# Performance work log

Hardware: AMD Instinct MI355X
Metric: run time of the kernel (lower is better)

The kernel has to match this reference:

```python
import jax, jax.numpy as jnp
import numpy as np

N, E = 20000, 160000
NODE_DIM, EDGE_DIM, H, STEPS = 64, 16, 32, 3


def setup_inputs() -> dict:
    key = jax.random.key(0)
    ks = jax.random.split(key, 10)
    node_feat = jax.random.normal(ks[0], (N, NODE_DIM), dtype=jnp.float32)
    edge_index = jax.random.randint(ks[1], (2, E), 0, N, dtype=jnp.int32)
    edge_feat = jax.random.normal(ks[2], (E, EDGE_DIM), dtype=jnp.float32)
    # node_proj: Linear(node_dim, hidden)
    W_np = jax.random.normal(ks[3], (H, NODE_DIM), dtype=jnp.float32) / np.sqrt(NODE_DIM)
    b_np = jnp.zeros((H,), dtype=jnp.float32)
    # edge_net: Linear(edge_dim, hidden*hidden) -> reshape [E, H, H]
    W_e = jax.random.normal(ks[4], (H * H, EDGE_DIM), dtype=jnp.float32) / np.sqrt(EDGE_DIM)
    b_e = jnp.zeros((H * H,), dtype=jnp.float32)
    # GRUCell params (torch layout: [3H, H], gate order r, z, n)
    W_ih = jax.random.normal(ks[5], (3 * H, H), dtype=jnp.float32) / np.sqrt(H)
    W_hh = jax.random.normal(ks[6], (3 * H, H), dtype=jnp.float32) / np.sqrt(H)
    b_ih = jnp.zeros((3 * H,), dtype=jnp.float32)
    b_hh = jnp.zeros((3 * H,), dtype=jnp.float32)
    return {
        "node_feat": node_feat, "edge_index": edge_index, "edge_feat": edge_feat,
        "W_np": W_np, "b_np": b_np, "W_e": W_e, "b_e": b_e,
        "W_ih": W_ih, "W_hh": W_hh, "b_ih": b_ih, "b_hh": b_hh,
    }


def _gru_cell(x, h, W_ih, W_hh, b_ih, b_hh):
    gi = x @ W_ih.T + b_ih  # [N, 3H]
    gh = h @ W_hh.T + b_hh
    ir, iz, inn = jnp.split(gi, 3, axis=-1)
    hr, hz, hn = jnp.split(gh, 3, axis=-1)
    r = jax.nn.sigmoid(ir + hr)
    z = jax.nn.sigmoid(iz + hz)
    n = jnp.tanh(inn + r * hn)
    return (1.0 - z) * n + z * h


def reference(node_feat, edge_index, edge_feat, W_np, b_np, W_e, b_e, W_ih, W_hh, b_ih, b_hh):
    h = node_feat @ W_np.T + b_np                      # [N, H]
    A = (edge_feat @ W_e.T + b_e).reshape(-1, H, H)    # [E, H, H] per-edge matrices
    src, dst = edge_index[0], edge_index[1]
    for _ in range(STEPS):
        # m[v] += A[e] @ h[src[e]]  -> batched matvec + scatter-add
        msg = jnp.einsum('ehk,ek->eh', A, h[src])      # [E, H]
        m = jax.ops.segment_sum(msg, dst, num_segments=N)
        h = _gru_cell(m, h, W_ih, W_hh, b_ih, b_hh)
    return h
```

## Files before the change

### kernel.cpp

```cpp
#include <hip/hip_runtime.h>
#include <math.h>

#define N_NODES 20000
#define N_EDGES 160000
#define NODE_DIM 64
#define EDGE_DIM 16
#define H 32
#define STEPS 3

__global__ void hist_src_kernel(const int* __restrict__ ei, int* __restrict__ deg) {
    int e = blockIdx.x * 256 + threadIdx.x;
    if (e < N_EDGES) atomicAdd(&deg[ei[e]], 1);
}

__global__ void scan_a_kernel(const int* __restrict__ deg,
                              int* __restrict__ part, int* __restrict__ bsum) {
    __shared__ int s[256];
    int v = blockIdx.x * 256 + threadIdx.x;
    int x = (v < N_NODES) ? deg[v] : 0;
    s[threadIdx.x] = x;
    __syncthreads();
    for (int off = 1; off < 256; off <<= 1) {
        int t = (threadIdx.x >= off) ? s[threadIdx.x - off] : 0;
        __syncthreads();
        s[threadIdx.x] += t;
        __syncthreads();
    }
    if (v < N_NODES) part[v] = s[threadIdx.x] - x;
    if (threadIdx.x == 255) bsum[blockIdx.x] = s[255];
}

__global__ void scan_b_kernel(int* __restrict__ rowptr,
                              const int* __restrict__ bsum,
                              int* __restrict__ cursor) {
    __shared__ int boff[80];
    if (threadIdx.x == 0) {
        int run = 0;
        for (int b = 0; b < 79; ++b) { boff[b] = run; run += bsum[b]; }
    }
    __syncthreads();
    for (int v = threadIdx.x; v < N_NODES; v += 256) {
        int r = rowptr[v] + boff[v >> 8];
        rowptr[v] = r;
        cursor[v] = r;
    }
    if (threadIdx.x == 0) rowptr[N_NODES] = N_EDGES;
}

__global__ void fill_src_kernel(const int* __restrict__ ei, int* __restrict__ cursor,
                                int* __restrict__ eperm, int2* __restrict__ sd2) {
    int e = blockIdx.x * 256 + threadIdx.x;
    if (e < N_EDGES) {
        int s = ei[e];
        int slot = atomicAdd(&cursor[s], 1);
        eperm[slot] = e;
        sd2[slot]   = make_int2(s, ei[N_EDGES + e]);
    }
}

__global__ void permute_ef_kernel(const float* __restrict__ ef,
                                  const int* __restrict__ eperm,
                                  float* __restrict__ ef2) {
    int t = blockIdx.x * 256 + threadIdx.x;
    if (t < N_EDGES * EDGE_DIM) {
        int j = t >> 4;
        int d = t & 15;
        ef2[t] = ef[eperm[j] * EDGE_DIM + d];
    }
}

__global__ void node_proj_kernel(const float* __restrict__ nf,
                                 const float* __restrict__ W,
                                 const float* __restrict__ b,
                                 float* __restrict__ h) {
    int tid = blockIdx.x * blockDim.x + threadIdx.x;
    if (tid >= N_NODES * H) return;
    int v = tid >> 5;
    int i = tid & 31;
    const float* __restrict__ row = nf + v * NODE_DIM;
    const float* __restrict__ w   = W + i * NODE_DIM;
    float acc = b[i];
#pragma unroll
    for (int d = 0; d < NODE_DIM; ++d) acc = fmaf(row[d], w[d], acc);
    h[tid] = acc;
}

__global__ __launch_bounds__(576)
void fused_msg_kernel(const float* __restrict__ We,
                      const float* __restrict__ be,
                      const float* __restrict__ h,
                      const int* __restrict__ rowptr,
                      const int2* __restrict__ sd2,
                      const float* __restrict__ ef2,
                      float* __restrict__ m) {
    __shared__ float hs[16 * 32];
    __shared__ float Ul[16 * 576];

    int t = threadIdx.x;

    float wreg[32];
    int p = -1;
    if (t < 512) {
        int L = t >> 4, q = (t >> 2) & 3, e = t & 3;
        int d = t & 15;
#pragma unroll
        for (int k = 0; k < H; ++k) wreg[k] = We[(L * H + k) * EDGE_DIM + d];
        p = q * 136 + L * 4 + e;
    } else if (t < 544) {
        int i = t - 512;
#pragma unroll
        for (int k = 0; k < H; ++k) wreg[k] = be[i * H + k];
        p = 544 + i;
    }

    int v0 = blockIdx.x * 16;

    if (t < 512) hs[t] = h[(size_t)v0 * H + t];
    __syncthreads();

    if (p >= 0) {
        for (int n = 0; n < 16; n += 2) {
            const float4* __restrict__ hp0 = (const float4*)(hs + n * H);
            const float4* __restrict__ hp1 = (const float4*)(hs + (n + 1) * H);
            float a0 = 0.f, a1 = 0.f;
#pragma unroll
            for (int kk = 0; kk < 8; ++kk) {
                float4 q0 = hp0[kk];
                float4 q1 = hp1[kk];
                a0 = fmaf(wreg[4 * kk + 0], q0.x, a0);
                a1 = fmaf(wreg[4 * kk + 0], q1.x, a1);
                a0 = fmaf(wreg[4 * kk + 1], q0.y, a0);
                a1 = fmaf(wreg[4 * kk + 1], q1.y, a1);
                a0 = fmaf(wreg[4 * kk + 2], q0.z, a0);
                a1 = fmaf(wreg[4 * kk + 2], q1.z, a1);
                a0 = fmaf(wreg[4 * kk + 3], q0.w, a0);
                a1 = fmaf(wreg[4 * kk + 3], q1.w, a1);
            }
            Ul[n * 576 + p]       = a0;
            Ul[(n + 1) * 576 + p] = a1;
        }
    }
    __syncthreads();

    int hw    = t >> 5;
    int lane  = t & 31;
    int jbeg  = rowptr[v0];
    int jend  = rowptr[v0 + 16];
    int nE    = jend - jbeg;
    int chunk = (nE + 17) / 18;
    int ja    = jbeg + hw * chunk;
    int jz    = ja + chunk; if (jz > jend) jz = jend;

    if (ja < jz) {
        int s_prev = -1;
        float4 u0 = {0,0,0,0}, u1 = {0,0,0,0}, u2 = {0,0,0,0}, u3 = {0,0,0,0};
        float  bv = 0.f;

        int2 sd = sd2[ja];
        const float4* __restrict__ ep0 = (const float4*)(ef2 + (size_t)ja * EDGE_DIM);
        float4 e0 = ep0[0], e1 = ep0[1], e2 = ep0[2], e3 = ep0[3];

        for (int j = ja; j < jz; ++j) {
            int jn = (j + 1 < jz) ? (j + 1) : j;
            int2 sdn = sd2[jn];
            const float4* __restrict__ epn =
                (const float4*)(ef2 + (size_t)jn * EDGE_DIM);
            float4 f0 = epn[0], f1 = epn[1], f2 = epn[2], f3 = epn[3];

            if (sd.x != s_prev) {
                s_prev = sd.x;
                int ls = sd.x - v0;
                const float4* __restrict__ up = (const float4*)(Ul + ls * 576);
                u0 = up[0 * 34 + lane];
                u1 = up[1 * 34 + lane];
                u2 = up[2 * 34 + lane];
                u3 = up[3 * 34 + lane];
                bv = Ul[ls * 576 + 544 + lane];
            }

            float msg = bv;
            msg = fmaf(e0.x, u0.x, msg);
            msg = fmaf(e0.y, u0.y, msg);
            msg = fmaf(e0.z, u0.z, msg);
            msg = fmaf(e0.w, u0.w, msg);
            msg = fmaf(e1.x, u1.x, msg);
            msg = fmaf(e1.y, u1.y, msg);
            msg = fmaf(e1.z, u1.z, msg);
            msg = fmaf(e1.w, u1.w, msg);
            msg = fmaf(e2.x, u2.x, msg);
            msg = fmaf(e2.y, u2.y, msg);
            msg = fmaf(e2.z, u2.z, msg);
            msg = fmaf(e2.w, u2.w, msg);
            msg = fmaf(e3.x, u3.x, msg);
            msg = fmaf(e3.y, u3.y, msg);
            msg = fmaf(e3.z, u3.z, msg);
            msg = fmaf(e3.w, u3.w, msg);

            atomicAdd(&m[(size_t)sd.y * H + lane], msg);

            sd = sdn;
            e0 = f0; e1 = f1; e2 = f2; e3 = f3;
        }
    }
}

__global__ __launch_bounds__(256, 4)
void gru_kernel(const float* __restrict__ Wih,
                const float* __restrict__ Whh,
                const float* __restrict__ bih,
                const float* __restrict__ bhh,
                float* __restrict__ m,
                const float* __restrict__ h,
                float* __restrict__ hout) {
    __shared__ float xs[16 * 64];
    __shared__ float gs[16 * 32 * 5];

    int c = threadIdx.x & 127;
    float4 wc[16];
    if (c < 96) {
        const float4* p = (const float4*)(Wih + c * H);
#pragma unroll
        for (int q = 0; q < 8; ++q) wc[q] = p[q];
    } else {
#pragma unroll
        for (int q = 0; q < 8; ++q) wc[q] = make_float4(0.f, 0.f, 0.f, 0.f);
    }
    int hrow = (c < 64) ? c : ((c >= 96) ? (c - 32) : -1);
    if (hrow >= 0) {
        const float4* p = (const float4*)(Whh + hrow * H);
#pragma unroll
        for (int q = 0; q < 8; ++q) wc[8 + q] = p[q];
    } else {
#pragma unroll
        for (int q = 0; q < 8; ++q) wc[8 + q] = make_float4(0.f, 0.f, 0.f, 0.f);
    }
    float bias;
    if (c < 64)      bias = bih[c] + bhh[c];
    else if (c < 96) bias = bih[c];
    else             bias = bhh[c - 32];

    int g    = threadIdx.x >> 5;
    int lane = threadIdx.x & 31;
    int half = threadIdx.x >> 7;
    int ci   = c & 31;
    int gt   = c >> 5;

    int v0 = blockIdx.x * 16;
    {
#pragma unroll
        for (int nn = 0; nn < 2; ++nn) {
            int n = g + nn * 8;
            int v = v0 + n;
            float mv = m[(size_t)v * H + lane];
            m[(size_t)v * H + lane] = 0.f;
            xs[n * 64 + lane]      = mv;
            xs[n * 64 + 32 + lane] = h[(size_t)v * H + lane];
        }
        __syncthreads();

#pragma unroll
        for (int n = 0; n < 8; n += 2) {
            const float4* x0 = (const float4*)(xs + (half * 8 + n) * 64);
            const float4* x1 = (const float4*)(xs + (half * 8 + n + 1) * 64);
            float acc0 = bias, acc1 = bias;
#pragma unroll
            for (int q = 0; q < 16; ++q) {
                float4 w = wc[q];
                float4 a = x0[q];
                float4 b = x1[q];
                acc0 = fmaf(w.x, a.x, acc0); acc1 = fmaf(w.x, b.x, acc1);
                acc0 = fmaf(w.y, a.y, acc0); acc1 = fmaf(w.y, b.y, acc1);
                acc0 = fmaf(w.z, a.z, acc0); acc1 = fmaf(w.z, b.z, acc1);
                acc0 = fmaf(w.w, a.w, acc0); acc1 = fmaf(w.w, b.w, acc1);
            }
            gs[((half * 8 + n)     * 32 + ci) * 5 + gt] = acc0;
            gs[((half * 8 + n + 1) * 32 + ci) * 5 + gt] = acc1;
        }
        __syncthreads();

        for (int t = threadIdx.x; t < 16 * 32; t += 256) {
            int nl = t >> 5, ii = t & 31;
            const float* gp = gs + (size_t)t * 5;
            float rs = gp[0], zs = gp[1], in_ = gp[2], hn = gp[3];
            float hv = xs[nl * 64 + 32 + ii];
            float r   = 1.f / (1.f + __expf(-rs));
            float z   = 1.f / (1.f + __expf(-zs));
            float nn2 = tanhf(in_ + r * hn);
            hout[(size_t)(v0 + nl) * H + ii] = (1.f - z) * nn2 + z * hv;
        }
    }
}

extern "C" void kernel_launch(void* const* d_in, const int* in_sizes, int n_in,
                              void* d_out, int out_size, void* d_ws, size_t ws_size,
                              hipStream_t stream) {
    const float* node_feat = (const float*)d_in[0];
    const int*   edge_idx  = (const int*)  d_in[1];
    const float* edge_feat = (const float*)d_in[2];
    const float* W_np      = (const float*)d_in[3];
    const float* b_np      = (const float*)d_in[4];
    const float* W_e       = (const float*)d_in[5];
    const float* b_e       = (const float*)d_in[6];
    const float* W_ih      = (const float*)d_in[7];
    const float* W_hh      = (const float*)d_in[8];
    const float* b_ih      = (const float*)d_in[9];
    const float* b_hh      = (const float*)d_in[10];

    float* h      = (float*)d_ws;
    float* m      = h + (size_t)N_NODES * H;
    float* ef2    = m + (size_t)N_NODES * H;
    int* rowptr   = (int*)(ef2 + (size_t)N_EDGES * EDGE_DIM);
    int* cursor   = rowptr + (N_NODES + 1);
    int* bsum     = cursor + N_NODES;
    int* eperm    = bsum + 80;
    int2* sd2     = (int2*)(eperm + N_EDGES);
    float* out    = (float*)d_out;

    hipMemsetAsync(m, 0, (size_t)N_NODES * H * sizeof(float), stream);
    hipMemsetAsync(cursor, 0, N_NODES * sizeof(int), stream);
    hist_src_kernel<<<(N_EDGES + 255) / 256, 256, 0, stream>>>(edge_idx, cursor);
    scan_a_kernel<<<(N_NODES + 255) / 256, 256, 0, stream>>>(cursor, rowptr, bsum);
    scan_b_kernel<<<1, 256, 0, stream>>>(rowptr, bsum, cursor);
    fill_src_kernel<<<(N_EDGES + 255) / 256, 256, 0, stream>>>(edge_idx, cursor,
                                                               eperm, sd2);
    permute_ef_kernel<<<(N_EDGES * EDGE_DIM + 255) / 256, 256, 0, stream>>>(
        edge_feat, eperm, ef2);

    node_proj_kernel<<<(N_NODES * H + 255) / 256, 256, 0, stream>>>(
        node_feat, W_np, b_np, h);

    for (int step = 0; step < STEPS; ++step) {
        fused_msg_kernel<<<N_NODES / 16, 576, 0, stream>>>(
            W_e, b_e, h, rowptr, sd2, ef2, m);
        float* dst_h = (step == STEPS - 1) ? out : h;
        gru_kernel<<<N_NODES / 16, 256, 0, stream>>>(W_ih, W_hh, b_ih, b_hh,
                                                     m, h, dst_h);
    }
}
```

Before: 302.8 us.

## Fuse setup kernels into one cooperative kernel; process two node tiles per message block

Replaces the two memsets and six preprocessing kernels with a single cooperative setup kernel. It uses grid.sync between the phases: zeroing plus node projection, source histogram, scan, offset fixup, CSR fill and edge-feature permute. The aim is to cut launch and inter-kernel gap overhead. The message kernel now handles two 16-node tiles per block, so the per-thread edge-net weight loads into registers are amortized over twice the work. The trade-offs are fewer message blocks, which means less parallelism, plus grid-wide barriers and a fixed 256-block grid for setup.

```diff
diff --git a/kernel.cpp b/kernel.cpp
--- a/kernel.cpp
+++ b/kernel.cpp
@@ -1,5 +1,8 @@
 #include <hip/hip_runtime.h>
+#include <hip/hip_cooperative_groups.h>
 #include <math.h>
+
+namespace cg = cooperative_groups;
 
 #define N_NODES 20000
 #define N_EDGES 160000
@@ -8,81 +11,95 @@
 #define H 32
 #define STEPS 3
 
-__global__ void hist_src_kernel(const int* __restrict__ ei, int* __restrict__ deg) {
-    int e = blockIdx.x * 256 + threadIdx.x;
-    if (e < N_EDGES) atomicAdd(&deg[ei[e]], 1);
-}
-
-__global__ void scan_a_kernel(const int* __restrict__ deg,
-                              int* __restrict__ part, int* __restrict__ bsum) {
+__global__ void setup_kernel(const int* __restrict__ ei,
+                             const float* __restrict__ ef,
+                             const float* __restrict__ nf,
+                             const float* __restrict__ W_np,
+                             const float* __restrict__ b_np,
+                             float* __restrict__ h,
+                             float* __restrict__ m,
+                             float* __restrict__ ef2,
+                             int* __restrict__ rowptr,
+                             int* __restrict__ cursor,
+                             int* __restrict__ bsum,
+                             int* __restrict__ eperm,
+                             int2* __restrict__ sd2) {
+    cg::grid_group grid = cg::this_grid();
     __shared__ int s[256];
-    int v = blockIdx.x * 256 + threadIdx.x;
-    int x = (v < N_NODES) ? deg[v] : 0;
-    s[threadIdx.x] = x;
-    __syncthreads();
-    for (int off = 1; off < 256; off <<= 1) {
-        int t = (threadIdx.x >= off) ? s[threadIdx.x - off] : 0;
-        __syncthreads();
-        s[threadIdx.x] += t;
-        __syncthreads();
-    }
-    if (v < N_NODES) part[v] = s[threadIdx.x] - x;
-    if (threadIdx.x == 255) bsum[blockIdx.x] = s[255];
-}
-
-__global__ void scan_b_kernel(int* __restrict__ rowptr,
-                              const int* __restrict__ bsum,
-                              int* __restrict__ cursor) {
     __shared__ int boff[80];
-    if (threadIdx.x == 0) {
-        int run = 0;
-        for (int b = 0; b < 79; ++b) { boff[b] = run; run += bsum[b]; }
-    }
-    __syncthreads();
-    for (int v = threadIdx.x; v < N_NODES; v += 256) {
-        int r = rowptr[v] + boff[v >> 8];
-        rowptr[v] = r;
-        cursor[v] = r;
-    }
-    if (threadIdx.x == 0) rowptr[N_NODES] = N_EDGES;
-}
-
-__global__ void fill_src_kernel(const int* __restrict__ ei, int* __restrict__ cursor,
-                                int* __restrict__ eperm, int2* __restrict__ sd2) {
-    int e = blockIdx.x * 256 + threadIdx.x;
-    if (e < N_EDGES) {
-        int s = ei[e];
-        int slot = atomicAdd(&cursor[s], 1);
+
+    const int tid = blockIdx.x * 256 + threadIdx.x;
+    const int nth = gridDim.x * 256;
+
+    {
+        float4* m4 = (float4*)m;
+        for (int i = tid; i < (N_NODES * H) / 4; i += nth)
+            m4[i] = make_float4(0.f, 0.f, 0.f, 0.f);
+        for (int i = tid; i < N_NODES; i += nth) cursor[i] = 0;
+        for (int t2 = tid; t2 < N_NODES * H; t2 += nth) {
+            int v = t2 >> 5;
+            int i = t2 & 31;
+            const float* __restrict__ row = nf + v * NODE_DIM;
+            const float* __restrict__ w   = W_np + i * NODE_DIM;
+            float acc = b_np[i];
+#pragma unroll
+            for (int d = 0; d < NODE_DIM; ++d) acc = fmaf(row[d], w[d], acc);
+            h[t2] = acc;
+        }
+    }
+    grid.sync();
+
+    for (int e = tid; e < N_EDGES; e += nth)
+        atomicAdd(&cursor[ei[e]], 1);
+    grid.sync();
+
+    if (blockIdx.x < 79) {
+        int v = blockIdx.x * 256 + threadIdx.x;
+        int x = (v < N_NODES) ? cursor[v] : 0;
+        s[threadIdx.x] = x;
+        __syncthreads();
+        for (int off = 1; off < 256; off <<= 1) {
+            int t = (threadIdx.x >= off) ? s[threadIdx.x - off] : 0;
+            __syncthreads();
+            s[threadIdx.x] += t;
+            __syncthreads();
+        }
+        if (v < N_NODES) rowptr[v] = s[threadIdx.x] - x;
+        if (threadIdx.x == 255) bsum[blockIdx.x] = s[255];
+    }
+    grid.sync();
+
+    if (blockIdx.x == 0) {
+        if (threadIdx.x == 0) {
+            int run = 0;
+            for (int b = 0; b < 79; ++b) { boff[b] = run; run += bsum[b]; }
+        }
+        __syncthreads();
+        for (int v = threadIdx.x; v < N_NODES; v += 256) {
+            int r = rowptr[v] + boff[v >> 8];
+            rowptr[v] = r;
+            cursor[v] = r;
+        }
+        if (threadIdx.x == 0) rowptr[N_NODES] = N_EDGES;
+    }
+    grid.sync();
+
+    for (int e = tid; e < N_EDGES; e += nth) {
+        int src = ei[e];
+        int slot = atomicAdd(&cursor[src], 1);
         eperm[slot] = e;
-        sd2[slot]   = make_int2(s, ei[N_EDGES + e]);
-    }
-}
-
-__global__ void permute_ef_kernel(const float* __restrict__ ef,
-                                  const int* __restrict__ eperm,
-                                  float* __restrict__ ef2) {
-    int t = blockIdx.x * 256 + threadIdx.x;
-    if (t < N_EDGES * EDGE_DIM) {
-        int j = t >> 4;
-        int d = t & 15;
-        ef2[t] = ef[eperm[j] * EDGE_DIM + d];
-    }
-}
-
-__global__ void node_proj_kernel(const float* __restrict__ nf,
-                                 const float* __restrict__ W,
-                                 const float* __restrict__ b,
-                                 float* __restrict__ h) {
-    int tid = blockIdx.x * blockDim.x + threadIdx.x;
-    if (tid >= N_NODES * H) return;
-    int v = tid >> 5;
-    int i = tid & 31;
-    const float* __restrict__ row = nf + v * NODE_DIM;
-    const float* __restrict__ w   = W + i * NODE_DIM;
-    float acc = b[i];
-#pragma unroll
-    for (int d = 0; d < NODE_DIM; ++d) acc = fmaf(row[d], w[d], acc);
-    h[tid] = acc;
+        sd2[slot]   = make_int2(src, ei[N_EDGES + e]);
+    }
+    grid.sync();
+
+    for (int j = tid; j < N_EDGES; j += nth) {
+        const float4* __restrict__ src = (const float4*)(ef + (size_t)eperm[j] * EDGE_DIM);
+        float4* __restrict__ dst       = (float4*)(ef2 + (size_t)j * EDGE_DIM);
+        dst[0] = src[0];
+        dst[1] = src[1];
+        dst[2] = src[2];
+        dst[3] = src[3];
+    }
 }
 
 __global__ __launch_bounds__(576)
@@ -113,94 +130,97 @@
         p = 544 + i;
     }
 
-    int v0 = blockIdx.x * 16;
-
-    if (t < 512) hs[t] = h[(size_t)v0 * H + t];
-    __syncthreads();
-
-    if (p >= 0) {
-        for (int n = 0; n < 16; n += 2) {
-            const float4* __restrict__ hp0 = (const float4*)(hs + n * H);
-            const float4* __restrict__ hp1 = (const float4*)(hs + (n + 1) * H);
-            float a0 = 0.f, a1 = 0.f;
-#pragma unroll
-            for (int kk = 0; kk < 8; ++kk) {
-                float4 q0 = hp0[kk];
-                float4 q1 = hp1[kk];
-                a0 = fmaf(wreg[4 * kk + 0], q0.x, a0);
-                a1 = fmaf(wreg[4 * kk + 0], q1.x, a1);
-                a0 = fmaf(wreg[4 * kk + 1], q0.y, a0);
-                a1 = fmaf(wreg[4 * kk + 1], q1.y, a1);
-                a0 = fmaf(wreg[4 * kk + 2], q0.z, a0);
-                a1 = fmaf(wreg[4 * kk + 2], q1.z, a1);
-                a0 = fmaf(wreg[4 * kk + 3], q0.w, a0);
-                a1 = fmaf(wreg[4 * kk + 3], q1.w, a1);
+    for (int tile = 0; tile < 2; ++tile) {
+        int v0 = (blockIdx.x * 2 + tile) * 16;
+
+        if (t < 512) hs[t] = h[(size_t)v0 * H + t];
+        __syncthreads();
+
+        if (p >= 0) {
+            for (int n = 0; n < 16; n += 2) {
+                const float4* __restrict__ hp0 = (const float4*)(hs + n * H);
+                const float4* __restrict__ hp1 = (const float4*)(hs + (n + 1) * H);
+                float a0 = 0.f, a1 = 0.f;
+#pragma unroll
+                for (int kk = 0; kk < 8; ++kk) {
+                    float4 q0 = hp0[kk];
+                    float4 q1 = hp1[kk];
+                    a0 = fmaf(wreg[4 * kk + 0], q0.x, a0);
+                    a1 = fmaf(wreg[4 * kk + 0], q1.x, a1);
+                    a0 = fmaf(wreg[4 * kk + 1], q0.y, a0);
+                    a1 = fmaf(wreg[4 * kk + 1], q1.y, a1);
+                    a0 = fmaf(wreg[4 * kk + 2], q0.z, a0);
+                    a1 = fmaf(wreg[4 * kk + 2], q1.z, a1);
+                    a0 = fmaf(wreg[4 * kk + 3], q0.w, a0);
+                    a1 = fmaf(wreg[4 * kk + 3], q1.w, a1);
+                }
+                Ul[n * 576 + p]       = a0;
+                Ul[(n + 1) * 576 + p] = a1;
             }
-            Ul[n * 576 + p]       = a0;
-            Ul[(n + 1) * 576 + p] = a1;
-        }
-    }
-    __syncthreads();
-
-    int hw    = t >> 5;
-    int lane  = t & 31;
-    int jbeg  = rowptr[v0];
-    int jend  = rowptr[v0 + 16];
-    int nE    = jend - jbeg;
-    int chunk = (nE + 17) / 18;
-    int ja    = jbeg + hw * chunk;
-    int jz    = ja + chunk; if (jz > jend) jz = jend;
-
-    if (ja < jz) {
-        int s_prev = -1;
-        float4 u0 = {0,0,0,0}, u1 = {0,0,0,0}, u2 = {0,0,0,0}, u3 = {0,0,0,0};
-        float  bv = 0.f;
-
-        int2 sd = sd2[ja];
-        const float4* __restrict__ ep0 = (const float4*)(ef2 + (size_t)ja * EDGE_DIM);
-        float4 e0 = ep0[0], e1 = ep0[1], e2 = ep0[2], e3 = ep0[3];
-
-        for (int j = ja; j < jz; ++j) {
-            int jn = (j + 1 < jz) ? (j + 1) : j;
-            int2 sdn = sd2[jn];
-            const float4* __restrict__ epn =
-                (const float4*)(ef2 + (size_t)jn * EDGE_DIM);
-            float4 f0 = epn[0], f1 = epn[1], f2 = epn[2], f3 = epn[3];
-
-            if (sd.x != s_prev) {
-                s_prev = sd.x;
-                int ls = sd.x - v0;
-                const float4* __restrict__ up = (const float4*)(Ul + ls * 576);
-                u0 = up[0 * 34 + lane];
-                u1 = up[1 * 34 + lane];
-                u2 = up[2 * 34 + lane];
-                u3 = up[3 * 34 + lane];
-                bv = Ul[ls * 576 + 544 + lane];
+        }
+        __syncthreads();
+
+        int hw    = t >> 5;
+        int lane  = t & 31;
+        int jbeg  = rowptr[v0];
+        int jend  = rowptr[v0 + 16];
+        int nE    = jend - jbeg;
+        int chunk = (nE + 17) / 18;
+        int ja    = jbeg + hw * chunk;
+        int jz    = ja + chunk; if (jz > jend) jz = jend;
+
+        if (ja < jz) {
+            int s_prev = -1;
+            float4 u0 = {0,0,0,0}, u1 = {0,0,0,0}, u2 = {0,0,0,0}, u3 = {0,0,0,0};
+            float  bv = 0.f;
+
+            int2 sd = sd2[ja];
+            const float4* __restrict__ ep0 = (const float4*)(ef2 + (size_t)ja * EDGE_DIM);
+            float4 e0 = ep0[0], e1 = ep0[1], e2 = ep0[2], e3 = ep0[3];
+
+            for (int j = ja; j < jz; ++j) {
+                int jn = (j + 1 < jz) ? (j + 1) : j;
+                int2 sdn = sd2[jn];
+                const float4* __restrict__ epn =
+                    (const float4*)(ef2 + (size_t)jn * EDGE_DIM);
+                float4 f0 = epn[0], f1 = epn[1], f2 = epn[2], f3 = epn[3];
+
+                if (sd.x != s_prev) {
+                    s_prev = sd.x;
+                    int ls = sd.x - v0;
+                    const float4* __restrict__ up = (const float4*)(Ul + ls * 576);
+                    u0 = up[0 * 34 + lane];
+                    u1 = up[1 * 34 + lane];
+                    u2 = up[2 * 34 + lane];
+                    u3 = up[3 * 34 + lane];
+                    bv = Ul[ls * 576 + 544 + lane];
+                }
+
+                float msg = bv;
+                msg = fmaf(e0.x, u0.x, msg);
+                msg = fmaf(e0.y, u0.y, msg);
+                msg = fmaf(e0.z, u0.z, msg);
+                msg = fmaf(e0.w, u0.w, msg);
+                msg = fmaf(e1.x, u1.x, msg);
+                msg = fmaf(e1.y, u1.y, msg);
+                msg = fmaf(e1.z, u1.z, msg);
+                msg = fmaf(e1.w, u1.w, msg);
+                msg = fmaf(e2.x, u2.x, msg);
+                msg = fmaf(e2.y, u2.y, msg);
+                msg = fmaf(e2.z, u2.z, msg);
+                msg = fmaf(e2.w, u2.w, msg);
+                msg = fmaf(e3.x, u3.x, msg);
+                msg = fmaf(e3.y, u3.y, msg);
+                msg = fmaf(e3.z, u3.z, msg);
+                msg = fmaf(e3.w, u3.w, msg);
+
+                atomicAdd(&m[(size_t)sd.y * H + lane], msg);
+
+                sd = sdn;
+                e0 = f0; e1 = f1; e2 = f2; e3 = f3;
             }
-
-            float msg = bv;
-            msg = fmaf(e0.x, u0.x, msg);
-            msg = fmaf(e0.y, u0.y, msg);
-            msg = fmaf(e0.z, u0.z, msg);
-            msg = fmaf(e0.w, u0.w, msg);
-            msg = fmaf(e1.x, u1.x, msg);
-            msg = fmaf(e1.y, u1.y, msg);
-            msg = fmaf(e1.z, u1.z, msg);
-            msg = fmaf(e1.w, u1.w, msg);
-            msg = fmaf(e2.x, u2.x, msg);
-            msg = fmaf(e2.y, u2.y, msg);
-            msg = fmaf(e2.z, u2.z, msg);
-            msg = fmaf(e2.w, u2.w, msg);
-            msg = fmaf(e3.x, u3.x, msg);
-            msg = fmaf(e3.y, u3.y, msg);
-            msg = fmaf(e3.z, u3.z, msg);
-            msg = fmaf(e3.w, u3.w, msg);
-
-            atomicAdd(&m[(size_t)sd.y * H + lane], msg);
-
-            sd = sdn;
-            e0 = f0; e1 = f1; e2 = f2; e3 = f3;
-        }
+        }
+        __syncthreads();
     }
 }
 
@@ -312,25 +332,22 @@
     int* rowptr   = (int*)(ef2 + (size_t)N_EDGES * EDGE_DIM);
     int* cursor   = rowptr + (N_NODES + 1);
     int* bsum     = cursor + N_NODES;
-    int* eperm    = bsum + 80;
+    int* eperm    = bsum + 81;
     int2* sd2     = (int2*)(eperm + N_EDGES);
     float* out    = (float*)d_out;
 
-    hipMemsetAsync(m, 0, (size_t)N_NODES * H * sizeof(float), stream);
-    hipMemsetAsync(cursor, 0, N_NODES * sizeof(int), stream);
-    hist_src_kernel<<<(N_EDGES + 255) / 256, 256, 0, stream>>>(edge_idx, cursor);
-    scan_a_kernel<<<(N_NODES + 255) / 256, 256, 0, stream>>>(cursor, rowptr, bsum);
-    scan_b_kernel<<<1, 256, 0, stream>>>(rowptr, bsum, cursor);
-    fill_src_kernel<<<(N_EDGES + 255) / 256, 256, 0, stream>>>(edge_idx, cursor,
-                                                               eperm, sd2);
-    permute_ef_kernel<<<(N_EDGES * EDGE_DIM + 255) / 256, 256, 0, stream>>>(
-        edge_feat, eperm, ef2);
-
-    node_proj_kernel<<<(N_NODES * H + 255) / 256, 256, 0, stream>>>(
-        node_feat, W_np, b_np, h);
+    void* args[] = {
+        (void*)&edge_idx, (void*)&edge_feat, (void*)&node_feat,
+        (void*)&W_np, (void*)&b_np,
+        (void*)&h, (void*)&m, (void*)&ef2,
+        (void*)&rowptr, (void*)&cursor, (void*)&bsum,
+        (void*)&eperm, (void*)&sd2
+    };
+    hipLaunchCooperativeKernel((void*)setup_kernel, dim3(256), dim3(256),
+                               args, 0, stream);
 
     for (int step = 0; step < STEPS; ++step) {
-        fused_msg_kernel<<<N_NODES / 16, 576, 0, stream>>>(
+        fused_msg_kernel<<<N_NODES / 32, 576, 0, stream>>>(
             W_e, b_e, h, rowptr, sd2, ef2, m);
         float* dst_h = (step == STEPS - 1) ? out : h;
         gru_kernel<<<N_NODES / 16, 256, 0, stream>>>(W_ih, W_hh, b_ih, b_hh,
```

After: 549.7 us. 1.82x slower.

## Replace atomic scatter-add with dst-sorted message buffer and segmented reduction in GRU

Applied to the files above, without the earlier changes.

Builds a second CSR keyed by destination and records, for each src-sorted edge, its slot in dst order. The message kernel writes each edge's message to that slot with a plain store instead of an atomicAdd into m. The GRU kernel then sums each node's contiguous run of messages itself. This removes float atomic contention and the zeroing of m, at the cost of a 20 MB per-edge message buffer written and read back each step, plus extra preprocessing atomics and scan work.

```diff
diff --git a/kernel.cpp b/kernel.cpp
--- a/kernel.cpp
+++ b/kernel.cpp
@@ -8,15 +8,27 @@
 #define H 32
 #define STEPS 3
 
-__global__ void hist_src_kernel(const int* __restrict__ ei, int* __restrict__ deg) {
+__global__ void hist_kernel(const int* __restrict__ ei,
+                            int* __restrict__ deg_s,
+                            int* __restrict__ deg_d) {
     int e = blockIdx.x * 256 + threadIdx.x;
-    if (e < N_EDGES) atomicAdd(&deg[ei[e]], 1);
-}
-
-__global__ void scan_a_kernel(const int* __restrict__ deg,
-                              int* __restrict__ part, int* __restrict__ bsum) {
+    if (e < N_EDGES) {
+        atomicAdd(&deg_s[ei[e]], 1);
+        atomicAdd(&deg_d[ei[N_EDGES + e]], 1);
+    }
+}
+
+__global__ void scan_a_kernel(const int* __restrict__ deg_s,
+                              const int* __restrict__ deg_d,
+                              int* __restrict__ part_s,
+                              int* __restrict__ part_d,
+                              int* __restrict__ bsum) {
     __shared__ int s[256];
-    int v = blockIdx.x * 256 + threadIdx.x;
+    int which = (blockIdx.x >= 79);
+    const int* __restrict__ deg = which ? deg_d : deg_s;
+    int* __restrict__ part      = which ? part_d : part_s;
+    int b = which ? (blockIdx.x - 79) : blockIdx.x;
+    int v = b * 256 + threadIdx.x;
     int x = (v < N_NODES) ? deg[v] : 0;
     s[threadIdx.x] = x;
     __syncthreads();
@@ -30,13 +42,19 @@
     if (threadIdx.x == 255) bsum[blockIdx.x] = s[255];
 }
 
-__global__ void scan_b_kernel(int* __restrict__ rowptr,
+__global__ void scan_b_kernel(int* __restrict__ rowptr_s,
+                              int* __restrict__ rowptr_d,
                               const int* __restrict__ bsum,
-                              int* __restrict__ cursor) {
+                              int* __restrict__ cursor_s,
+                              int* __restrict__ cursor_d) {
     __shared__ int boff[80];
+    int which = blockIdx.x;
+    int* __restrict__ rowptr = which ? rowptr_d : rowptr_s;
+    int* __restrict__ cursor = which ? cursor_d : cursor_s;
+    const int* __restrict__ bs = bsum + which * 79;
     if (threadIdx.x == 0) {
         int run = 0;
-        for (int b = 0; b < 79; ++b) { boff[b] = run; run += bsum[b]; }
+        for (int b = 0; b < 79; ++b) { boff[b] = run; run += bs[b]; }
     }
     __syncthreads();
     for (int v = threadIdx.x; v < N_NODES; v += 256) {
@@ -47,14 +65,19 @@
     if (threadIdx.x == 0) rowptr[N_NODES] = N_EDGES;
 }
 
-__global__ void fill_src_kernel(const int* __restrict__ ei, int* __restrict__ cursor,
-                                int* __restrict__ eperm, int2* __restrict__ sd2) {
+__global__ void fill_kernel(const int* __restrict__ ei,
+                            int* __restrict__ cursor_s,
+                            int* __restrict__ cursor_d,
+                            int* __restrict__ eperm,
+                            int2* __restrict__ ss2) {
     int e = blockIdx.x * 256 + threadIdx.x;
     if (e < N_EDGES) {
         int s = ei[e];
-        int slot = atomicAdd(&cursor[s], 1);
+        int d = ei[N_EDGES + e];
+        int slot   = atomicAdd(&cursor_s[s], 1);
+        int slot_d = atomicAdd(&cursor_d[d], 1);
         eperm[slot] = e;
-        sd2[slot]   = make_int2(s, ei[N_EDGES + e]);
+        ss2[slot]   = make_int2(s, slot_d);
     }
 }
 
@@ -90,9 +113,9 @@
                       const float* __restrict__ be,
                       const float* __restrict__ h,
                       const int* __restrict__ rowptr,
-                      const int2* __restrict__ sd2,
+                      const int2* __restrict__ ss2,
                       const float* __restrict__ ef2,
-                      float* __restrict__ m) {
+                      float* __restrict__ msg_out) {
     __shared__ float hs[16 * 32];
     __shared__ float Ul[16 * 576];
 
@@ -156,20 +179,20 @@
         float4 u0 = {0,0,0,0}, u1 = {0,0,0,0}, u2 = {0,0,0,0}, u3 = {0,0,0,0};
         float  bv = 0.f;
 
-        int2 sd = sd2[ja];
+        int2 ss = ss2[ja];
         const float4* __restrict__ ep0 = (const float4*)(ef2 + (size_t)ja * EDGE_DIM);
         float4 e0 = ep0[0], e1 = ep0[1], e2 = ep0[2], e3 = ep0[3];
 
         for (int j = ja; j < jz; ++j) {
             int jn = (j + 1 < jz) ? (j + 1) : j;
-            int2 sdn = sd2[jn];
+            int2 ssn = ss2[jn];
             const float4* __restrict__ epn =
                 (const float4*)(ef2 + (size_t)jn * EDGE_DIM);
             float4 f0 = epn[0], f1 = epn[1], f2 = epn[2], f3 = epn[3];
 
-            if (sd.x != s_prev) {
-                s_prev = sd.x;
-                int ls = sd.x - v0;
+            if (ss.x != s_prev) {
+                s_prev = ss.x;
+                int ls = ss.x - v0;
                 const float4* __restrict__ up = (const float4*)(Ul + ls * 576);
                 u0 = up[0 * 34 + lane];
                 u1 = up[1 * 34 + lane];
@@ -196,9 +219,9 @@
             msg = fmaf(e3.z, u3.z, msg);
             msg = fmaf(e3.w, u3.w, msg);
 
-            atomicAdd(&m[(size_t)sd.y * H + lane], msg);
-
-            sd = sdn;
+            msg_out[(size_t)ss.y * H + lane] = msg;
+
+            ss = ssn;
             e0 = f0; e1 = f1; e2 = f2; e3 = f3;
         }
     }
@@ -209,7 +232,8 @@
                 const float* __restrict__ Whh,
                 const float* __restrict__ bih,
                 const float* __restrict__ bhh,
-                float* __restrict__ m,
+                const float* __restrict__ msg,
+                const int* __restrict__ rowptr_d,
                 const float* __restrict__ h,
                 float* __restrict__ hout) {
     __shared__ float xs[16 * 64];
@@ -251,9 +275,21 @@
         for (int nn = 0; nn < 2; ++nn) {
             int n = g + nn * 8;
             int v = v0 + n;
-            float mv = m[(size_t)v * H + lane];
-            m[(size_t)v * H + lane] = 0.f;
-            xs[n * 64 + lane]      = mv;
+            int beg = rowptr_d[v], end = rowptr_d[v + 1];
+            int cnt = end - beg;
+            const float* __restrict__ mp = msg + (size_t)beg * H + lane;
+            float a0 = 0.f, a1 = 0.f, a2 = 0.f, a3 = 0.f;
+            int pp = 0;
+            for (; pp + 4 <= cnt; pp += 4) {
+                float x0 = mp[0 * H];
+                float x1 = mp[1 * H];
+                float x2 = mp[2 * H];
+                float x3 = mp[3 * H];
+                a0 += x0; a1 += x1; a2 += x2; a3 += x3;
+                mp += 4 * H;
+            }
+            for (; pp < cnt; ++pp) { a0 += mp[0]; mp += H; }
+            xs[n * 64 + lane]      = (a0 + a1) + (a2 + a3);
             xs[n * 64 + 32 + lane] = h[(size_t)v * H + lane];
         }
         __syncthreads();
@@ -306,34 +342,37 @@
     const float* b_ih      = (const float*)d_in[9];
     const float* b_hh      = (const float*)d_in[10];
 
-    float* h      = (float*)d_ws;
-    float* m      = h + (size_t)N_NODES * H;
-    float* ef2    = m + (size_t)N_NODES * H;
-    int* rowptr   = (int*)(ef2 + (size_t)N_EDGES * EDGE_DIM);
-    int* cursor   = rowptr + (N_NODES + 1);
-    int* bsum     = cursor + N_NODES;
-    int* eperm    = bsum + 80;
-    int2* sd2     = (int2*)(eperm + N_EDGES);
-    float* out    = (float*)d_out;
-
-    hipMemsetAsync(m, 0, (size_t)N_NODES * H * sizeof(float), stream);
-    hipMemsetAsync(cursor, 0, N_NODES * sizeof(int), stream);
-    hist_src_kernel<<<(N_EDGES + 255) / 256, 256, 0, stream>>>(edge_idx, cursor);
-    scan_a_kernel<<<(N_NODES + 255) / 256, 256, 0, stream>>>(cursor, rowptr, bsum);
-    scan_b_kernel<<<1, 256, 0, stream>>>(rowptr, bsum, cursor);
-    fill_src_kernel<<<(N_EDGES + 255) / 256, 256, 0, stream>>>(edge_idx, cursor,
-                                                               eperm, sd2);
+    float* h       = (float*)d_ws;
+    float* msg     = h + (size_t)N_NODES * H;
+    float* ef2     = msg + (size_t)N_EDGES * H;
+    int* rowptr_s  = (int*)(ef2 + (size_t)N_EDGES * EDGE_DIM);
+    int* rowptr_d  = rowptr_s + (N_NODES + 1);
+    int* cursor_s  = rowptr_d + (N_NODES + 1);
+    int* cursor_d  = cursor_s + N_NODES;
+    int* bsum      = cursor_d + N_NODES;
+    int* eperm     = bsum + 160;
+    int2* ss2      = (int2*)(eperm + N_EDGES);
+    float* out     = (float*)d_out;
+
+    hipMemsetAsync(cursor_s, 0, 2 * N_NODES * sizeof(int), stream);
+    hist_kernel<<<(N_EDGES + 255) / 256, 256, 0, stream>>>(edge_idx,
+                                                           cursor_s, cursor_d);
+    scan_a_kernel<<<158, 256, 0, stream>>>(cursor_s, cursor_d,
+                                           rowptr_s, rowptr_d, bsum);
+    scan_b_kernel<<<2, 256, 0, stream>>>(rowptr_s, rowptr_d, bsum,
+                                         cursor_s, cursor_d);
+    fill_kernel<<<(N_EDGES + 255) / 256, 256, 0, stream>>>(edge_idx, cursor_s,
+                                                           cursor_d, eperm, ss2);
     permute_ef_kernel<<<(N_EDGES * EDGE_DIM + 255) / 256, 256, 0, stream>>>(
         edge_feat, eperm, ef2);
-
     node_proj_kernel<<<(N_NODES * H + 255) / 256, 256, 0, stream>>>(
         node_feat, W_np, b_np, h);
 
     for (int step = 0; step < STEPS; ++step) {
         fused_msg_kernel<<<N_NODES / 16, 576, 0, stream>>>(
-            W_e, b_e, h, rowptr, sd2, ef2, m);
+            W_e, b_e, h, rowptr_s, ss2, ef2, msg);
         float* dst_h = (step == STEPS - 1) ? out : h;
         gru_kernel<<<N_NODES / 16, 256, 0, stream>>>(W_ih, W_hh, b_ih, b_hh,
-                                                     m, h, dst_h);
-    }
-}
+                                                     msg, rowptr_d, h, dst_h);
+    }
+}
```

Result: slower. 333.9 us (+10.3%).
